# Kernel optimization log

Hardware: AMD Instinct MI355X
Metric: run time of the kernel (lower is better)

The kernel has to match this reference:

```python
import jax, jax.numpy as jnp
import numpy as np

N = 4096
IN_F = 256
OUT_F = 64
HEADS = 4
NEG_SLOPE = 0.2


def setup_inputs() -> dict:
    key = jax.random.key(0)
    k1, k2, k3, k4 = jax.random.split(key, 4)
    x = jax.random.normal(k1, (N, IN_F), dtype=jnp.float32)
    W = jax.random.normal(k2, (HEADS, IN_F, OUT_F), dtype=jnp.float32) * (1.0 / np.sqrt(IN_F))
    a = jax.random.normal(k3, (HEADS, 2 * OUT_F), dtype=jnp.float32) * (1.0 / np.sqrt(2 * OUT_F))
    adj_matrix = jax.random.randint(k4, (N, N), 0, 2, dtype=jnp.int32)
    return {"x": x, "W": W, "a": a, "adj_matrix": adj_matrix}


def reference(x, W, a, adj_matrix):
    heads, in_f, out_f = W.shape
    n = x.shape[0]
    # per-head linear transform: [H, N, F]
    xt = jnp.einsum('ni,hio->hno', x, W)
    # attention logit decomposes: a . cat(xt_i, xt_j) = src_i + dst_j
    src = jnp.einsum('hnf,hf->hn', xt, a[:, :out_f])   # [H, N]
    dst = jnp.einsum('hnf,hf->hn', xt, a[:, out_f:])   # [H, N]
    e = jax.nn.leaky_relu(src[:, :, None] + dst[:, None, :], NEG_SLOPE)  # [H, N, N]
    mask = (adj_matrix > 0)[None, :, :]
    e = jnp.where(mask, e, -jnp.inf)
    attention = jax.nn.softmax(e, axis=2)              # [H, N, N]
    # (dropout is identity in eval / p=0)
    h_prime = jnp.einsum('hij,hjf->hif', attention, xt)  # [H, N, F]
    # concat heads: [N, H*F]
    return h_prime.transpose(1, 0, 2).reshape(n, heads * out_f)
```

## Files before the change

kernel.cpp:

```cpp
#include <hip/hip_runtime.h>
#include <math.h>

#define N 4096
#define IN_F 256
#define OUT_F 64
#define HEADS 4
#define NEG 0.2f
#define JSPLIT 4

typedef float f32x4 __attribute__((ext_vector_type(4)));
typedef short short8 __attribute__((ext_vector_type(8)));

#define FMA4S(A, s, V) do { (A).x = fmaf((s),(V).x,(A).x); (A).y = fmaf((s),(V).y,(A).y); \
                            (A).z = fmaf((s),(V).z,(A).z); (A).w = fmaf((s),(V).w,(A).w); } while(0)

__device__ __forceinline__ unsigned short f2bf(float x) {
  unsigned int u = __float_as_uint(x);
  u += 0x7fffu + ((u >> 16) & 1u);
  return (unsigned short)(u >> 16);
}

__global__ __launch_bounds__(256) void k_xt(const float* __restrict__ x,
                                            const float* __restrict__ W,
                                            const float* __restrict__ a,
                                            short* __restrict__ xtB,
                                            float* __restrict__ src,
                                            float* __restrict__ dst) {
  __shared__ __align__(16) float xls[64 * 68];
  __shared__ __align__(16) float wls[64 * 64];
  const int t  = threadIdx.x;
  const int h  = blockIdx.y;
  const int i0 = blockIdx.x * 64;
  const int fg = t & 15;
  const int rg = t >> 4;

  float4 acc[4];
  acc[0] = acc[1] = acc[2] = acc[3] = make_float4(0.f, 0.f, 0.f, 0.f);

  const float4* xg = (const float4*)x;
  const float4* wg = (const float4*)W;
  float4* xls4 = (float4*)xls;
  float4* wls4 = (float4*)wls;
  const float4* xr4 = (const float4*)xls;
  const float4* wr4 = (const float4*)wls;

  for (int kt = 0; kt < 4; ++kt) {
    __syncthreads();
    #pragma unroll
    for (int s = 0; s < 4; ++s) {
      int f4i = t + 256 * s;
      int row = f4i >> 4, c4 = f4i & 15;
      xls4[row * 17 + c4] = xg[(size_t)(i0 + row) * 64 + kt * 16 + c4];
    }
    #pragma unroll
    for (int s = 0; s < 4; ++s) {
      int f4i = t + 256 * s;
      int kk = f4i >> 4, c4 = f4i & 15;
      wls4[kk * 16 + c4] = wg[(size_t)(h * 256 + kt * 64 + kk) * 16 + c4];
    }
    __syncthreads();
    #pragma unroll 4
    for (int kk = 0; kk < 64; kk += 4) {
      float4 wv0 = wr4[(kk + 0) * 16 + fg];
      float4 wv1 = wr4[(kk + 1) * 16 + fg];
      float4 wv2 = wr4[(kk + 2) * 16 + fg];
      float4 wv3 = wr4[(kk + 3) * 16 + fg];
      #pragma unroll
      for (int q = 0; q < 4; ++q) {
        float4 xv = xr4[(rg * 4 + q) * 17 + (kk >> 2)];
        FMA4S(acc[q], xv.x, wv0);
        FMA4S(acc[q], xv.y, wv1);
        FMA4S(acc[q], xv.z, wv2);
        FMA4S(acc[q], xv.w, wv3);
      }
    }
  }

  const float4* a4 = (const float4*)a;
  float4 as = a4[h * 32 + fg];
  float4 ad = a4[h * 32 + 16 + fg];
  #pragma unroll
  for (int q = 0; q < 4; ++q) {
    float s_ = acc[q].x * as.x + acc[q].y * as.y + acc[q].z * as.z + acc[q].w * as.w;
    float d_ = acc[q].x * ad.x + acc[q].y * ad.y + acc[q].z * ad.z + acc[q].w * ad.w;
    #pragma unroll
    for (int off = 1; off < 16; off <<= 1) {
      s_ += __shfl_xor(s_, off, 64);
      d_ += __shfl_xor(d_, off, 64);
    }
    if (fg == 0) {
      int r = rg * 4 + q;
      src[h * N + i0 + r] = s_;
      dst[h * N + i0 + r] = d_;
    }
  }

  __syncthreads();
  #pragma unroll
  for (int q = 0; q < 4; ++q) {
    *(float4*)&xls[(rg * 4 + q) * 68 + fg * 4] = acc[q];
  }
  __syncthreads();

  {
    const int lane = t & 63;
    const int g    = t >> 6;
    const int q    = lane >> 4;
    const int m    = lane & 15;
    short8* xb8 = (short8*)xtB;
    #pragma unroll
    for (int jcl = 0; jcl < 2; ++jcl) {
      int jc = (i0 >> 5) + jcl;
      short8 bv;
      #pragma unroll
      for (int r = 0; r < 8; ++r) {
        bv[r] = (short)f2bf(xls[(jcl * 32 + q * 8 + r) * 68 + g * 16 + m]);
      }
      xb8[((size_t)(h * 128 + jc) * 4 + g) * 64 + lane] = bv;
    }
  }
}

__global__ __launch_bounds__(256) void k_zero(float4* __restrict__ p, int n4) {
  int i = blockIdx.x * 256 + threadIdx.x;
  if (i < n4) p[i] = make_float4(0.f, 0.f, 0.f, 0.f);
}

__global__ __launch_bounds__(256) void k_flash(const int* __restrict__ adj,
                                               const float* __restrict__ src,
                                               const float* __restrict__ dst,
                                               const short* __restrict__ xtB,
                                               float* __restrict__ accG,
                                               float* __restrict__ lG) {
  const int t    = threadIdx.x;
  const int lane = t & 63;
  const int h    = t >> 6;
  const int i0   = blockIdx.x * 32;
  const int js   = blockIdx.y;
  const int q    = lane >> 4;
  const int m    = lane & 15;
  const int koff = q * 8;

  float sv = (lane < 32) ? src[h * N + i0 + lane] : 0.f;
  const float s0 = __shfl(sv, m, 64);
  const float s1 = __shfl(sv, 16 + m, 64);

  f32x4 acc0[4], acc1[4];
  #pragma unroll
  for (int g = 0; g < 4; ++g) { acc0[g] = (f32x4)(0.f); acc1[g] = (f32x4)(0.f); }
  float l0 = 0.f, l1 = 0.f;

  const short8* xb8 = (const short8*)xtB;
  const int jbase = js * (N / JSPLIT);

  for (int c = 0; c < (N / JSPLIT) / 32; ++c) {
    const int j0 = jbase + c * 32;

    union { float4 v[2]; float f[8]; } du;
    du.v[0] = *(const float4*)(dst + h * N + j0 + koff);
    du.v[1] = *(const float4*)(dst + h * N + j0 + koff + 4);

    union { int4 v[2]; int i[8]; } ad0, ad1;
    const int* r0 = adj + (size_t)(i0 + m) * N + j0 + koff;
    const int* r1 = adj + (size_t)(i0 + 16 + m) * N + j0 + koff;
    ad0.v[0] = *(const int4*)r0;  ad0.v[1] = *(const int4*)(r0 + 4);
    ad1.v[0] = *(const int4*)r1;  ad1.v[1] = *(const int4*)(r1 + 4);

    short8 b0 = xb8[((size_t)(h * 128 + (j0 >> 5)) * 4 + 0) * 64 + lane];
    short8 b1 = xb8[((size_t)(h * 128 + (j0 >> 5)) * 4 + 1) * 64 + lane];
    short8 b2 = xb8[((size_t)(h * 128 + (j0 >> 5)) * 4 + 2) * 64 + lane];
    short8 b3 = xb8[((size_t)(h * 128 + (j0 >> 5)) * 4 + 3) * 64 + lane];

    short8 a0, a1;
    #pragma unroll
    for (int r = 0; r < 8; ++r) {
      float e0 = s0 + du.f[r];
      e0 = fmaxf(e0, NEG * e0);
      float p0 = (ad0.i[r] > 0) ? __expf(e0) : 0.f;
      l0 += p0;
      a0[r] = (short)f2bf(p0);
      float e1 = s1 + du.f[r];
      e1 = fmaxf(e1, NEG * e1);
      float p1 = (ad1.i[r] > 0) ? __expf(e1) : 0.f;
      l1 += p1;
      a1[r] = (short)f2bf(p1);
    }

    acc0[0] = __builtin_amdgcn_mfma_f32_16x16x32_bf16(a0, b0, acc0[0], 0, 0, 0);
    acc0[1] = __builtin_amdgcn_mfma_f32_16x16x32_bf16(a0, b1, acc0[1], 0, 0, 0);
    acc0[2] = __builtin_amdgcn_mfma_f32_16x16x32_bf16(a0, b2, acc0[2], 0, 0, 0);
    acc0[3] = __builtin_amdgcn_mfma_f32_16x16x32_bf16(a0, b3, acc0[3], 0, 0, 0);
    acc1[0] = __builtin_amdgcn_mfma_f32_16x16x32_bf16(a1, b0, acc1[0], 0, 0, 0);
    acc1[1] = __builtin_amdgcn_mfma_f32_16x16x32_bf16(a1, b1, acc1[1], 0, 0, 0);
    acc1[2] = __builtin_amdgcn_mfma_f32_16x16x32_bf16(a1, b2, acc1[2], 0, 0, 0);
    acc1[3] = __builtin_amdgcn_mfma_f32_16x16x32_bf16(a1, b3, acc1[3], 0, 0, 0);
  }

  l0 += __shfl_xor(l0, 16, 64);  l0 += __shfl_xor(l0, 32, 64);
  l1 += __shfl_xor(l1, 16, 64);  l1 += __shfl_xor(l1, 32, 64);
  if (lane < 16) {
    atomicAdd(&lG[h * N + i0 + lane], l0);
    atomicAdd(&lG[h * N + i0 + 16 + lane], l1);
  }

  #pragma unroll
  for (int reg = 0; reg < 4; ++reg) {
    int row0 = i0 + q * 4 + reg;
    int row1 = row0 + 16;
    #pragma unroll
    for (int g = 0; g < 4; ++g) {
      atomicAdd(&accG[((size_t)h * N + row0) * 64 + g * 16 + m], acc0[g][reg]);
      atomicAdd(&accG[((size_t)h * N + row1) * 64 + g * 16 + m], acc1[g][reg]);
    }
  }
}

__global__ __launch_bounds__(256) void k_div(const float* __restrict__ accG,
                                             const float* __restrict__ lG,
                                             float* __restrict__ out) {
  int v = blockIdx.x * 256 + threadIdx.x;
  int col4 = v & 63;
  int i    = v >> 6;
  int h    = col4 >> 4;
  int fg   = col4 & 15;
  const float4* a4 = (const float4*)accG;
  float4 av = a4[((size_t)h * N + i) * 16 + fg];
  float il = 1.f / lG[h * N + i];
  float4 ov = make_float4(av.x * il, av.y * il, av.z * il, av.w * il);
  ((float4*)out)[v] = ov;
}

extern "C" void kernel_launch(void* const* d_in, const int* in_sizes, int n_in,
                              void* d_out, int out_size, void* d_ws, size_t ws_size,
                              hipStream_t stream) {
  const float* x   = (const float*)d_in[0];
  const float* W   = (const float*)d_in[1];
  const float* a   = (const float*)d_in[2];
  const int*   adj = (const int*)d_in[3];
  float* out = (float*)d_out;

  float* ws   = (float*)d_ws;
  short* xtB  = (short*)ws;
  float* src  = ws + 524288;
  float* dst  = src + HEADS * N;
  float* accG = dst + HEADS * N;
  float* lG   = accG + (size_t)HEADS * N * OUT_F;

  const int zero_n4 = (HEADS * N * OUT_F + HEADS * N) / 4;
  k_zero<<<dim3((zero_n4 + 255) / 256), 256, 0, stream>>>((float4*)accG, zero_n4);
  k_xt<<<dim3(64, 4), 256, 0, stream>>>(x, W, a, xtB, src, dst);
  k_flash<<<dim3(128, JSPLIT), 256, 0, stream>>>(adj, src, dst, xtB, accG, lG);
  k_div<<<dim3((N * OUT_F) / 256), 256, 0, stream>>>(accG, lG, out);
}
```

Baseline: 157.3 us.

## Use exp2 with prescaled logits, cheaper bf16 packing, more j-splits, restructure k_xt

Logits are prescaled by log2(e) in k_xt so the flash loop can call the hardware exp2 directly. Masked entries now get a large negative logit instead of a select after the exponential. Two bf16 values are packed with a single perm using round-half-up instead of per-element round-to-nearest-even. JSPLIT doubles to 8 for more blocks in k_flash, which doubles the atomic traffic into the accumulators. k_xt switches to 32-row tiles that read W straight from global memory with no LDS staging, and it launches twice as many blocks.

```diff
diff --git a/kernel.cpp b/kernel.cpp
--- a/kernel.cpp
+++ b/kernel.cpp
@@ -6,7 +6,8 @@
 #define OUT_F 64
 #define HEADS 4
 #define NEG 0.2f
-#define JSPLIT 4
+#define JSPLIT 8
+#define LOG2E 1.44269504088896f
 
 typedef float f32x4 __attribute__((ext_vector_type(4)));
 typedef short short8 __attribute__((ext_vector_type(8)));
@@ -18,6 +19,20 @@
   unsigned int u = __float_as_uint(x);
   u += 0x7fffu + ((u >> 16) & 1u);
   return (unsigned short)(u >> 16);
+}
+
+__device__ __forceinline__ float exp2_fast(float x) {
+#if __has_builtin(__builtin_amdgcn_exp2f)
+  return __builtin_amdgcn_exp2f(x);
+#else
+  return exp2f(x);
+#endif
+}
+
+__device__ __forceinline__ int pack_bf2(float p0, float p1) {
+  unsigned u0 = __float_as_uint(p0) + 0x8000u;
+  unsigned u1 = __float_as_uint(p1) + 0x8000u;
+  return (int)__builtin_amdgcn_perm(u1, u0, 0x07060302u);
 }
 
 __global__ __launch_bounds__(256) void k_xt(const float* __restrict__ x,
@@ -26,61 +41,52 @@
                                             short* __restrict__ xtB,
                                             float* __restrict__ src,
                                             float* __restrict__ dst) {
-  __shared__ __align__(16) float xls[64 * 68];
-  __shared__ __align__(16) float wls[64 * 64];
+  __shared__ __align__(16) float xls[32 * 260];
   const int t  = threadIdx.x;
   const int h  = blockIdx.y;
-  const int i0 = blockIdx.x * 64;
+  const int i0 = blockIdx.x * 32;
   const int fg = t & 15;
   const int rg = t >> 4;
 
-  float4 acc[4];
-  acc[0] = acc[1] = acc[2] = acc[3] = make_float4(0.f, 0.f, 0.f, 0.f);
-
   const float4* xg = (const float4*)x;
-  const float4* wg = (const float4*)W;
   float4* xls4 = (float4*)xls;
-  float4* wls4 = (float4*)wls;
   const float4* xr4 = (const float4*)xls;
-  const float4* wr4 = (const float4*)wls;
-
-  for (int kt = 0; kt < 4; ++kt) {
-    __syncthreads();
-    #pragma unroll
-    for (int s = 0; s < 4; ++s) {
-      int f4i = t + 256 * s;
-      int row = f4i >> 4, c4 = f4i & 15;
-      xls4[row * 17 + c4] = xg[(size_t)(i0 + row) * 64 + kt * 16 + c4];
-    }
-    #pragma unroll
-    for (int s = 0; s < 4; ++s) {
-      int f4i = t + 256 * s;
-      int kk = f4i >> 4, c4 = f4i & 15;
-      wls4[kk * 16 + c4] = wg[(size_t)(h * 256 + kt * 64 + kk) * 16 + c4];
-    }
-    __syncthreads();
-    #pragma unroll 4
-    for (int kk = 0; kk < 64; kk += 4) {
-      float4 wv0 = wr4[(kk + 0) * 16 + fg];
-      float4 wv1 = wr4[(kk + 1) * 16 + fg];
-      float4 wv2 = wr4[(kk + 2) * 16 + fg];
-      float4 wv3 = wr4[(kk + 3) * 16 + fg];
-      #pragma unroll
-      for (int q = 0; q < 4; ++q) {
-        float4 xv = xr4[(rg * 4 + q) * 17 + (kk >> 2)];
-        FMA4S(acc[q], xv.x, wv0);
-        FMA4S(acc[q], xv.y, wv1);
-        FMA4S(acc[q], xv.z, wv2);
-        FMA4S(acc[q], xv.w, wv3);
-      }
+
+  #pragma unroll
+  for (int s = 0; s < 8; ++s) {
+    int f4i = t + 256 * s;
+    int row = f4i >> 6, c4 = f4i & 63;
+    xls4[row * 65 + c4] = xg[(size_t)(i0 + row) * 64 + c4];
+  }
+  __syncthreads();
+
+  float4 acc[2];
+  acc[0] = acc[1] = make_float4(0.f, 0.f, 0.f, 0.f);
+  const float4* wg4 = (const float4*)W + (size_t)h * 256 * 16;
+
+  #pragma unroll 2
+  for (int kk = 0; kk < 256; kk += 4) {
+    float4 wv0 = wg4[(kk + 0) * 16 + fg];
+    float4 wv1 = wg4[(kk + 1) * 16 + fg];
+    float4 wv2 = wg4[(kk + 2) * 16 + fg];
+    float4 wv3 = wg4[(kk + 3) * 16 + fg];
+    #pragma unroll
+    for (int q = 0; q < 2; ++q) {
+      float4 xv = xr4[(rg * 2 + q) * 65 + (kk >> 2)];
+      FMA4S(acc[q], xv.x, wv0);
+      FMA4S(acc[q], xv.y, wv1);
+      FMA4S(acc[q], xv.z, wv2);
+      FMA4S(acc[q], xv.w, wv3);
     }
   }
 
   const float4* a4 = (const float4*)a;
   float4 as = a4[h * 32 + fg];
   float4 ad = a4[h * 32 + 16 + fg];
-  #pragma unroll
-  for (int q = 0; q < 4; ++q) {
+  as.x *= LOG2E; as.y *= LOG2E; as.z *= LOG2E; as.w *= LOG2E;
+  ad.x *= LOG2E; ad.y *= LOG2E; ad.z *= LOG2E; ad.w *= LOG2E;
+  #pragma unroll
+  for (int q = 0; q < 2; ++q) {
     float s_ = acc[q].x * as.x + acc[q].y * as.y + acc[q].z * as.z + acc[q].w * as.w;
     float d_ = acc[q].x * ad.x + acc[q].y * ad.y + acc[q].z * ad.z + acc[q].w * ad.w;
     #pragma unroll
@@ -89,7 +95,7 @@
       d_ += __shfl_xor(d_, off, 64);
     }
     if (fg == 0) {
-      int r = rg * 4 + q;
+      int r = rg * 2 + q;
       src[h * N + i0 + r] = s_;
       dst[h * N + i0 + r] = d_;
     }
@@ -97,8 +103,8 @@
 
   __syncthreads();
   #pragma unroll
-  for (int q = 0; q < 4; ++q) {
-    *(float4*)&xls[(rg * 4 + q) * 68 + fg * 4] = acc[q];
+  for (int q = 0; q < 2; ++q) {
+    *(float4*)&xls[(rg * 2 + q) * 68 + fg * 4] = acc[q];
   }
   __syncthreads();
 
@@ -107,17 +113,12 @@
     const int g    = t >> 6;
     const int q    = lane >> 4;
     const int m    = lane & 15;
-    short8* xb8 = (short8*)xtB;
-    #pragma unroll
-    for (int jcl = 0; jcl < 2; ++jcl) {
-      int jc = (i0 >> 5) + jcl;
-      short8 bv;
-      #pragma unroll
-      for (int r = 0; r < 8; ++r) {
-        bv[r] = (short)f2bf(xls[(jcl * 32 + q * 8 + r) * 68 + g * 16 + m]);
-      }
-      xb8[((size_t)(h * 128 + jc) * 4 + g) * 64 + lane] = bv;
-    }
+    short8 bv;
+    #pragma unroll
+    for (int r = 0; r < 8; ++r) {
+      bv[r] = (short)f2bf(xls[(q * 8 + r) * 68 + g * 16 + m]);
+    }
+    ((short8*)xtB)[((size_t)(h * 128 + blockIdx.x) * 4 + g) * 64 + lane] = bv;
   }
 }
 
@@ -153,6 +154,7 @@
   const short8* xb8 = (const short8*)xtB;
   const int jbase = js * (N / JSPLIT);
 
+  #pragma unroll 2
   for (int c = 0; c < (N / JSPLIT) / 32; ++c) {
     const int j0 = jbase + c * 32;
 
@@ -166,25 +168,43 @@
     ad0.v[0] = *(const int4*)r0;  ad0.v[1] = *(const int4*)(r0 + 4);
     ad1.v[0] = *(const int4*)r1;  ad1.v[1] = *(const int4*)(r1 + 4);
 
-    short8 b0 = xb8[((size_t)(h * 128 + (j0 >> 5)) * 4 + 0) * 64 + lane];
-    short8 b1 = xb8[((size_t)(h * 128 + (j0 >> 5)) * 4 + 1) * 64 + lane];
-    short8 b2 = xb8[((size_t)(h * 128 + (j0 >> 5)) * 4 + 2) * 64 + lane];
-    short8 b3 = xb8[((size_t)(h * 128 + (j0 >> 5)) * 4 + 3) * 64 + lane];
-
-    short8 a0, a1;
-    #pragma unroll
-    for (int r = 0; r < 8; ++r) {
-      float e0 = s0 + du.f[r];
-      e0 = fmaxf(e0, NEG * e0);
-      float p0 = (ad0.i[r] > 0) ? __expf(e0) : 0.f;
-      l0 += p0;
-      a0[r] = (short)f2bf(p0);
-      float e1 = s1 + du.f[r];
-      e1 = fmaxf(e1, NEG * e1);
-      float p1 = (ad1.i[r] > 0) ? __expf(e1) : 0.f;
-      l1 += p1;
-      a1[r] = (short)f2bf(p1);
-    }
+    const size_t bbase = ((size_t)(h * 128 + (j0 >> 5)) * 4) * 64 + lane;
+    short8 b0 = xb8[bbase + 0 * 64];
+    short8 b1 = xb8[bbase + 1 * 64];
+    short8 b2 = xb8[bbase + 2 * 64];
+    short8 b3 = xb8[bbase + 3 * 64];
+
+    int av0[4], av1[4];
+    #pragma unroll
+    for (int r2 = 0; r2 < 4; ++r2) {
+      float p0a, p0b, p1a, p1b;
+      {
+        float e = s0 + du.f[2 * r2];
+        float el = fmaxf(e, NEG * e);
+        el = (ad0.i[2 * r2] > 0) ? el : -1e30f;
+        p0a = exp2_fast(el);
+        float e2 = s0 + du.f[2 * r2 + 1];
+        float el2 = fmaxf(e2, NEG * e2);
+        el2 = (ad0.i[2 * r2 + 1] > 0) ? el2 : -1e30f;
+        p0b = exp2_fast(el2);
+      }
+      {
+        float e = s1 + du.f[2 * r2];
+        float el = fmaxf(e, NEG * e);
+        el = (ad1.i[2 * r2] > 0) ? el : -1e30f;
+        p1a = exp2_fast(el);
+        float e2 = s1 + du.f[2 * r2 + 1];
+        float el2 = fmaxf(e2, NEG * e2);
+        el2 = (ad1.i[2 * r2 + 1] > 0) ? el2 : -1e30f;
+        p1b = exp2_fast(el2);
+      }
+      l0 += p0a + p0b;
+      l1 += p1a + p1b;
+      av0[r2] = pack_bf2(p0a, p0b);
+      av1[r2] = pack_bf2(p1a, p1b);
+    }
+    short8 a0 = __builtin_bit_cast(short8, *(int4*)av0);
+    short8 a1 = __builtin_bit_cast(short8, *(int4*)av1);
 
     acc0[0] = __builtin_amdgcn_mfma_f32_16x16x32_bf16(a0, b0, acc0[0], 0, 0, 0);
     acc0[1] = __builtin_amdgcn_mfma_f32_16x16x32_bf16(a0, b1, acc0[1], 0, 0, 0);
@@ -248,7 +268,7 @@
 
   const int zero_n4 = (HEADS * N * OUT_F + HEADS * N) / 4;
   k_zero<<<dim3((zero_n4 + 255) / 256), 256, 0, stream>>>((float4*)accG, zero_n4);
-  k_xt<<<dim3(64, 4), 256, 0, stream>>>(x, W, a, xtB, src, dst);
+  k_xt<<<dim3(128, 4), 256, 0, stream>>>(x, W, a, xtB, src, dst);
   k_flash<<<dim3(128, JSPLIT), 256, 0, stream>>>(adj, src, dst, xtB, accG, lG);
   k_div<<<dim3((N * OUT_F) / 256), 256, 0, stream>>>(accG, lG, out);
 }
```

Measured after the change: 174.8 us. 1.11x slower.
